# Performance work log

Hardware: AMD Instinct MI355X
Metric: run time of the kernel (lower is better)

Reference implementation:

```python
import jax, jax.numpy as jnp
import numpy as np

TEMPERATURE = 0.1
BASE_TEMPERATURE = 0.1
COS_EPS = 1e-8  # torch.nn.CosineSimilarity default eps
BSZ, N_VIEWS, C = 8192, 1, 256
NUM_CLASSES = 1000


def setup_inputs() -> dict:
    key = jax.random.key(0)
    k1, k2 = jax.random.split(key)
    features = jax.random.normal(k1, (BSZ, N_VIEWS, C), dtype=jnp.float32)
    # int32 used (jax default x64 disabled); values are class ids in [0, NUM_CLASSES)
    labels = jax.random.randint(k2, (BSZ, N_VIEWS), 0, NUM_CLASSES, dtype=jnp.int32)
    return {"features": features, "labels": labels}


def reference(features, labels):
    # features: [bsz, n_views=1, C]; n_views==1 is the only shape-consistent case
    n = features.shape[0] * features.shape[1]
    f = features.reshape(n, -1)                       # contrast_feature == anchor_feature, [N, C]
    lab = labels.reshape(-1)                          # [N]

    # SupCon mask: mask_{ij} = 1 if same class
    mask = (lab[:, None] == lab[None, :]).astype(jnp.float32)   # [N, N]
    perfect_logit = jnp.where(mask == 1, 1.0, -1.0)

    # cosine similarity via L2-normalize + GEMM (same math as broadcasted CosineSimilarity)
    norms = jnp.linalg.norm(f, axis=-1, keepdims=True)
    fn = f / jnp.maximum(norms, COS_EPS)              # [N, C]
    logits = jnp.matmul(fn, fn.T) / TEMPERATURE       # [N, N]

    # logits_mask: ones with zeroed diagonal (exclude self-contrast)
    logits_mask = 1.0 - jnp.eye(n, dtype=jnp.float32)
    pos_mask = mask * logits_mask

    # faithful (unshifted) masked log-sum-exp, as in cal_log_prob
    denom = jnp.sum(jnp.exp(logits) * logits_mask, axis=1, keepdims=True)
    log_prob = logits - jnp.log(denom)                # [N, N]

    mean_log_prob_pos = jnp.sum(pos_mask * log_prob, axis=1) / (jnp.sum(pos_mask, axis=1) + 1e-6)
    loss = jnp.mean(-(TEMPERATURE / BASE_TEMPERATURE) * mean_log_prob_pos)
    return (loss, logits, perfect_logit)
```

## Files before the change

### kernel.cpp

```cpp
#include <hip/hip_runtime.h>
#include <hip/hip_bf16.h>

#define N 8192
#define C 256
#define NCLS 1000

typedef __bf16 bf16x8 __attribute__((ext_vector_type(8)));
typedef float floatx4 __attribute__((ext_vector_type(4)));

__device__ __forceinline__ void gload_lds16(const void* g, void* l) {
    __builtin_amdgcn_global_load_lds(
        (const __attribute__((address_space(1))) void*)g,
        (__attribute__((address_space(3))) void*)l, 16, 0, 0);
}

__device__ __forceinline__ unsigned short f2bf(float x) {
    union { float f; unsigned int u; } a; a.f = x;
    unsigned int u = a.u;
    unsigned int r = (u + 0x7fffu + ((u >> 16) & 1u)) >> 16;
    return (unsigned short)r;
}

__global__ __launch_bounds__(256) void k_norm(const float* __restrict__ f,
                                              unsigned short* __restrict__ fnb) {
    int wid = threadIdx.x >> 6, lane = threadIdx.x & 63;
    int row = blockIdx.x * 4 + wid;
    const float4* fr = (const float4*)(f + (size_t)row * C);
    float4 v = fr[lane];
    float ss = v.x * v.x + v.y * v.y + v.z * v.z + v.w * v.w;
    #pragma unroll
    for (int m = 1; m < 64; m <<= 1) ss += __shfl_xor(ss, m, 64);
    float scale = 1.0f / fmaxf(sqrtf(ss), 1e-8f);
    ushort4 o;
    o.x = f2bf(v.x * scale); o.y = f2bf(v.y * scale);
    o.z = f2bf(v.z * scale); o.w = f2bf(v.w * scale);
    ((ushort4*)(fnb + (size_t)row * C))[lane] = o;
}

__global__ __launch_bounds__(1024) void k_hist(const int* __restrict__ lab,
                                               int* __restrict__ cnt) {
    __shared__ int bins[NCLS];
    for (int i = threadIdx.x; i < NCLS; i += 1024) bins[i] = 0;
    __syncthreads();
    for (int i = threadIdx.x; i < N; i += 1024) atomicAdd(&bins[lab[i]], 1);
    __syncthreads();
    for (int i = threadIdx.x; i < NCLS; i += 1024) cnt[i] = bins[i];
}

__global__ __launch_bounds__(256) void k_perfect(const int* __restrict__ lab,
                                                 float* __restrict__ perfect) {
    __shared__ int labs[N];
    const int t = threadIdx.x;
    #pragma unroll
    for (int p = 0; p < N / (256 * 4); ++p) {
        int idx = (p * 256 + t) * 4;
        int4 v = *(const int4*)(lab + idx);
        *(int4*)&labs[idx] = v;
    }
    __syncthreads();
    int row0 = blockIdx.x * 4;
    #pragma unroll
    for (int rr = 0; rr < 4; ++rr) {
        int row = row0 + rr;
        int lr = labs[row];
        float* dst = perfect + (size_t)row * N;
        #pragma unroll
        for (int p = 0; p < 8; ++p) {
            int c = (p * 256 + t) * 4;
            floatx4 pv;
            pv[0] = (labs[c + 0] == lr) ? 1.0f : -1.0f;
            pv[1] = (labs[c + 1] == lr) ? 1.0f : -1.0f;
            pv[2] = (labs[c + 2] == lr) ? 1.0f : -1.0f;
            pv[3] = (labs[c + 3] == lr) ? 1.0f : -1.0f;
            *(floatx4*)(dst + c) = pv;
        }
    }
}

__global__ __launch_bounds__(256) void k_gemm(
    const unsigned short* __restrict__ fnb, const int* __restrict__ lab,
    float* __restrict__ logits,
    float* __restrict__ Ssum, float* __restrict__ Psum) {
    const int bx = blockIdx.x, by = blockIdx.y;
    if (bx < by) return;
    const bool diag = (bx == by);

    __shared__ __align__(16) char smem[16896];
    unsigned short* As = (unsigned short*)smem;
    unsigned short* Bs = (unsigned short*)(smem + 8192);
    float* T = (float*)smem;
    __shared__ __align__(16) int Lr[128];
    __shared__ __align__(16) int Lc[128];

    const int t = threadIdx.x;
    const int wid = t >> 6, lane = t & 63;
    const int waveM = wid >> 1, waveN = wid & 1;
    const int quad = lane >> 4, l15 = lane & 15;
    const int rowBase = by * 128;
    const int colBase = bx * 128;

    if (t < 128) Lr[t] = lab[rowBase + t];
    else         Lc[t - 128] = lab[colBase + (t - 128)];

    floatx4 acc[4][4] = {};

    const int srow = wid * 16 + (lane >> 2);
    const int scol = (lane & 3) * 8;
    const unsigned short* gA = fnb + (size_t)(rowBase + srow) * C + scol;
    const unsigned short* gB = fnb + (size_t)(colBase + srow) * C + scol;
    char* asb = (char*)As + wid * 1024;
    char* bsb = (char*)Bs + wid * 1024;

    for (int kb = 0; kb < C; kb += 32) {
        __syncthreads();
        gload_lds16(gA + kb,           asb);
        gload_lds16(gA + kb + 64 * C,  asb + 4096);
        gload_lds16(gB + kb,           bsb);
        gload_lds16(gB + kb + 64 * C,  bsb + 4096);
        __syncthreads();
        bf16x8 a[4], b[4];
        #pragma unroll
        for (int i = 0; i < 4; ++i) {
            a[i] = *(const bf16x8*)&As[(waveM * 64 + i * 16 + l15) * 32 + quad * 8];
            b[i] = *(const bf16x8*)&Bs[(waveN * 64 + i * 16 + l15) * 32 + quad * 8];
        }
        #pragma unroll
        for (int i = 0; i < 4; ++i)
            #pragma unroll
            for (int j = 0; j < 4; ++j)
                acc[i][j] = __builtin_amdgcn_mfma_f32_16x16x32_bf16(a[i], b[j], acc[i][j], 0, 0, 0);
    }

    const float invT = 10.0f;
    float colS[4] = {0.f, 0.f, 0.f, 0.f};
    float colP[4] = {0.f, 0.f, 0.f, 0.f};

    #pragma unroll
    for (int i = 0; i < 4; ++i) {
        #pragma unroll
        for (int r = 0; r < 4; ++r) {
            int lrow = waveM * 64 + i * 16 + quad * 4 + r;
            int row = rowBase + lrow;
            int labr = Lr[lrow];
            float eS = 0.f, pS = 0.f;
            #pragma unroll
            for (int j = 0; j < 4; ++j) {
                int lcol = waveN * 64 + j * 16 + l15;
                int col = colBase + lcol;
                float v = acc[i][j][r] * invT;
                size_t off = (size_t)row * N + col;
                bool same = (labr == Lc[lcol]);
                logits[off] = v;
                if (!diag || row != col) {
                    float e = __expf(v);
                    eS += e;
                    if (same) pS += v;
                    if (!diag) {
                        colS[j] += e;
                        if (same) colP[j] += v;
                    }
                }
            }
            #pragma unroll
            for (int m = 1; m < 16; m <<= 1) {
                eS += __shfl_xor(eS, m, 64);
                pS += __shfl_xor(pS, m, 64);
            }
            if (l15 == 0) {
                atomicAdd(&Ssum[row], eS);
                if (pS != 0.0f) atomicAdd(&Psum[row], pS);
            }
        }
    }

    if (!diag) {
        #pragma unroll
        for (int j = 0; j < 4; ++j) {
            float cs = colS[j], cp = colP[j];
            cs += __shfl_xor(cs, 16, 64); cs += __shfl_xor(cs, 32, 64);
            cp += __shfl_xor(cp, 16, 64); cp += __shfl_xor(cp, 32, 64);
            if (quad == 0) {
                int col = colBase + waveN * 64 + j * 16 + l15;
                atomicAdd(&Ssum[col], cs);
                if (cp != 0.0f) atomicAdd(&Psum[col], cp);
            }
        }

        #pragma unroll
        for (int c = 0; c < 4; ++c) {
            __syncthreads();
            if (waveN == (c >> 1)) {
                #pragma unroll
                for (int jj = 0; jj < 2; ++jj) {
                    int j = (c & 1) * 2 + jj;
                    int tr = jj * 16 + l15;
                    #pragma unroll
                    for (int i = 0; i < 4; ++i) {
                        floatx4 w;
                        w[0] = acc[i][j][0] * invT; w[1] = acc[i][j][1] * invT;
                        w[2] = acc[i][j][2] * invT; w[3] = acc[i][j][3] * invT;
                        *(floatx4*)&T[tr * 132 + waveM * 64 + i * 16 + quad * 4] = w;
                    }
                }
            }
            __syncthreads();
            #pragma unroll
            for (int pass = 0; pass < 4; ++pass) {
                int rr = pass * 8 + (t >> 5);
                int cv = (t & 31) * 4;
                floatx4 lv = *(const floatx4*)&T[rr * 132 + cv];
                size_t off = (size_t)(colBase + c * 32 + rr) * N + rowBase + cv;
                *(floatx4*)(logits + off) = lv;
            }
        }
    }
}

__global__ __launch_bounds__(1024) void k_loss(
    const float* __restrict__ S, const float* __restrict__ P,
    const int* __restrict__ lab, const int* __restrict__ cnt,
    float* __restrict__ out) {
    float sum = 0.f;
    for (int i = threadIdx.x; i < N; i += 1024) {
        float Ki = (float)(cnt[lab[i]] - 1);
        float term = (P[i] - Ki * logf(S[i])) / (Ki + 1e-6f);
        sum += term;
    }
    #pragma unroll
    for (int m = 1; m < 64; m <<= 1) sum += __shfl_xor(sum, m, 64);
    __shared__ float wsum[16];
    int wid = threadIdx.x >> 6, lane = threadIdx.x & 63;
    if (lane == 0) wsum[wid] = sum;
    __syncthreads();
    if (threadIdx.x == 0) {
        float tot = 0.f;
        #pragma unroll
        for (int i = 0; i < 16; ++i) tot += wsum[i];
        out[0] = -tot / (float)N;
    }
}

extern "C" void kernel_launch(void* const* d_in, const int* in_sizes, int n_in,
                              void* d_out, int out_size, void* d_ws, size_t ws_size,
                              hipStream_t stream) {
    const float* f = (const float*)d_in[0];
    const int* lab = (const int*)d_in[1];
    float* out = (float*)d_out;
    float* logits = out + 1;
    float* perfect = out + 1 + (size_t)N * N;

    unsigned short* fnb = (unsigned short*)d_ws;
    float* Ssum = (float*)((char*)d_ws + (size_t)N * C * 2);
    float* Psum = Ssum + N;
    int* cnt = (int*)(Psum + N);

    hipMemsetAsync(Ssum, 0, 2 * N * sizeof(float), stream);
    k_perfect<<<N / 4, 256, 0, stream>>>(lab, perfect);
    k_norm<<<N / 4, 256, 0, stream>>>(f, fnb);
    k_hist<<<1, 1024, 0, stream>>>(lab, cnt);
    k_gemm<<<dim3(64, 64), 256, 0, stream>>>(fnb, lab, logits, Ssum, Psum);
    k_loss<<<1, 1024, 0, stream>>>(Ssum, Psum, lab, cnt, out);
}
```

Baseline: 626.4 us.

## Double-buffer GEMM LDS loads, launch only triangular tiles, widen perfect-logit rows

The GEMM kernel now double-buffers its LDS tiles, so the next K-slice's global-to-LDS load is issued while the MFMAs run on the current one, and it needs one barrier per iteration instead of two. It also launches exactly the 2080 upper-triangular tiles, mapping a linear block index to (bx,by) with a sqrt and fixup loops, instead of launching 4096 blocks where half exit immediately. The perfect-logit kernel handles 8 rows per block and reuses one int4 label load across those 8 rows. LDS use doubles to 32 KB, which could lower occupancy.

```diff
diff --git a/kernel.cpp b/kernel.cpp
--- a/kernel.cpp
+++ b/kernel.cpp
@@ -49,30 +49,30 @@
 
 __global__ __launch_bounds__(256) void k_perfect(const int* __restrict__ lab,
                                                  float* __restrict__ perfect) {
-    __shared__ int labs[N];
+    __shared__ __align__(16) int labs[N];
     const int t = threadIdx.x;
     #pragma unroll
-    for (int p = 0; p < N / (256 * 4); ++p) {
+    for (int p = 0; p < 8; ++p) {
         int idx = (p * 256 + t) * 4;
-        int4 v = *(const int4*)(lab + idx);
-        *(int4*)&labs[idx] = v;
-    }
-    __syncthreads();
-    int row0 = blockIdx.x * 4;
-    #pragma unroll
-    for (int rr = 0; rr < 4; ++rr) {
-        int row = row0 + rr;
-        int lr = labs[row];
-        float* dst = perfect + (size_t)row * N;
-        #pragma unroll
-        for (int p = 0; p < 8; ++p) {
-            int c = (p * 256 + t) * 4;
+        *(int4*)&labs[idx] = *(const int4*)(lab + idx);
+    }
+    __syncthreads();
+    const int row0 = blockIdx.x * 8;
+    int lr[8];
+    #pragma unroll
+    for (int rr = 0; rr < 8; ++rr) lr[rr] = labs[row0 + rr];
+    #pragma unroll
+    for (int p = 0; p < 8; ++p) {
+        int c = (p * 256 + t) * 4;
+        int4 lv = *(const int4*)&labs[c];
+        #pragma unroll
+        for (int rr = 0; rr < 8; ++rr) {
             floatx4 pv;
-            pv[0] = (labs[c + 0] == lr) ? 1.0f : -1.0f;
-            pv[1] = (labs[c + 1] == lr) ? 1.0f : -1.0f;
-            pv[2] = (labs[c + 2] == lr) ? 1.0f : -1.0f;
-            pv[3] = (labs[c + 3] == lr) ? 1.0f : -1.0f;
-            *(floatx4*)(dst + c) = pv;
+            pv[0] = (lv.x == lr[rr]) ? 1.0f : -1.0f;
+            pv[1] = (lv.y == lr[rr]) ? 1.0f : -1.0f;
+            pv[2] = (lv.z == lr[rr]) ? 1.0f : -1.0f;
+            pv[3] = (lv.w == lr[rr]) ? 1.0f : -1.0f;
+            *(floatx4*)(perfect + (size_t)(row0 + rr) * N + c) = pv;
         }
     }
 }
@@ -81,13 +81,14 @@
     const unsigned short* __restrict__ fnb, const int* __restrict__ lab,
     float* __restrict__ logits,
     float* __restrict__ Ssum, float* __restrict__ Psum) {
-    const int bx = blockIdx.x, by = blockIdx.y;
-    if (bx < by) return;
+    int k = blockIdx.x;
+    int r = (int)((sqrtf(8.0f * (float)k + 1.0f) - 1.0f) * 0.5f);
+    while ((r + 1) * (r + 2) / 2 <= k) ++r;
+    while (r * (r + 1) / 2 > k) --r;
+    const int bx = r, by = k - r * (r + 1) / 2;
     const bool diag = (bx == by);
 
-    __shared__ __align__(16) char smem[16896];
-    unsigned short* As = (unsigned short*)smem;
-    unsigned short* Bs = (unsigned short*)(smem + 8192);
+    __shared__ __align__(16) char smem[32768];
     float* T = (float*)smem;
     __shared__ __align__(16) int Lr[128];
     __shared__ __align__(16) int Lc[128];
@@ -108,28 +109,38 @@
     const int scol = (lane & 3) * 8;
     const unsigned short* gA = fnb + (size_t)(rowBase + srow) * C + scol;
     const unsigned short* gB = fnb + (size_t)(colBase + srow) * C + scol;
-    char* asb = (char*)As + wid * 1024;
-    char* bsb = (char*)Bs + wid * 1024;
-
-    for (int kb = 0; kb < C; kb += 32) {
-        __syncthreads();
-        gload_lds16(gA + kb,           asb);
-        gload_lds16(gA + kb + 64 * C,  asb + 4096);
-        gload_lds16(gB + kb,           bsb);
-        gload_lds16(gB + kb + 64 * C,  bsb + 4096);
-        __syncthreads();
+
+    #define STAGE(buf, kb) do {                                   \
+        char* asb = smem + (buf) * 16384 + wid * 1024;            \
+        char* bsb = asb + 8192;                                   \
+        gload_lds16(gA + (kb),          asb);                     \
+        gload_lds16(gA + (kb) + 64 * C, asb + 4096);              \
+        gload_lds16(gB + (kb),          bsb);                     \
+        gload_lds16(gB + (kb) + 64 * C, bsb + 4096);              \
+    } while (0)
+
+    STAGE(0, 0);
+    __syncthreads();
+    #pragma unroll
+    for (int it = 0; it < 8; ++it) {
+        const int cur = it & 1;
+        if (it < 7) STAGE(cur ^ 1, (it + 1) * 32);
+        const unsigned short* Ab = (const unsigned short*)(smem + cur * 16384);
+        const unsigned short* Bb = Ab + 4096;
         bf16x8 a[4], b[4];
         #pragma unroll
         for (int i = 0; i < 4; ++i) {
-            a[i] = *(const bf16x8*)&As[(waveM * 64 + i * 16 + l15) * 32 + quad * 8];
-            b[i] = *(const bf16x8*)&Bs[(waveN * 64 + i * 16 + l15) * 32 + quad * 8];
+            a[i] = *(const bf16x8*)&Ab[(waveM * 64 + i * 16 + l15) * 32 + quad * 8];
+            b[i] = *(const bf16x8*)&Bb[(waveN * 64 + i * 16 + l15) * 32 + quad * 8];
         }
         #pragma unroll
         for (int i = 0; i < 4; ++i)
             #pragma unroll
             for (int j = 0; j < 4; ++j)
                 acc[i][j] = __builtin_amdgcn_mfma_f32_16x16x32_bf16(a[i], b[j], acc[i][j], 0, 0, 0);
-    }
+        __syncthreads();
+    }
+    #undef STAGE
 
     const float invT = 10.0f;
     float colS[4] = {0.f, 0.f, 0.f, 0.f};
@@ -138,8 +149,8 @@
     #pragma unroll
     for (int i = 0; i < 4; ++i) {
         #pragma unroll
-        for (int r = 0; r < 4; ++r) {
-            int lrow = waveM * 64 + i * 16 + quad * 4 + r;
+        for (int r2 = 0; r2 < 4; ++r2) {
+            int lrow = waveM * 64 + i * 16 + quad * 4 + r2;
             int row = rowBase + lrow;
             int labr = Lr[lrow];
             float eS = 0.f, pS = 0.f;
@@ -147,7 +158,7 @@
             for (int j = 0; j < 4; ++j) {
                 int lcol = waveN * 64 + j * 16 + l15;
                 int col = colBase + lcol;
-                float v = acc[i][j][r] * invT;
+                float v = acc[i][j][r2] * invT;
                 size_t off = (size_t)row * N + col;
                 bool same = (labr == Lc[lcol]);
                 logits[off] = v;
@@ -255,9 +266,9 @@
     int* cnt = (int*)(Psum + N);
 
     hipMemsetAsync(Ssum, 0, 2 * N * sizeof(float), stream);
-    k_perfect<<<N / 4, 256, 0, stream>>>(lab, perfect);
+    k_perfect<<<N / 8, 256, 0, stream>>>(lab, perfect);
     k_norm<<<N / 4, 256, 0, stream>>>(f, fnb);
     k_hist<<<1, 1024, 0, stream>>>(lab, cnt);
-    k_gemm<<<dim3(64, 64), 256, 0, stream>>>(fnb, lab, logits, Ssum, Psum);
+    k_gemm<<<2080, 256, 0, stream>>>(fnb, lab, logits, Ssum, Psum);
     k_loss<<<1, 1024, 0, stream>>>(Ssum, Psum, lab, cnt, out);
 }
```

After: 632.0 us. No clear change (+0.9%).
